# Optimization experiments

Hardware: AMD Instinct MI355X
Metric: run time of the kernel (lower is better)

Reference implementation:

```python
import jax, jax.numpy as jnp
import numpy as np

B, N, D, H, IN, HID = 16, 1024, 256, 8, 256, 1024
HD = IN // H  # head dim = 32
EPS = 1e-5


def layer_norm(x, g, b):
    mu = jnp.mean(x, axis=-1, keepdims=True)
    var = jnp.var(x, axis=-1, keepdims=True)
    return (x - mu) / jnp.sqrt(var + EPS) * g + b


def setup_inputs() -> dict:
    key = jax.random.key(0)
    ks = jax.random.split(key, 12)
    s = 0.02
    return {
        "x": jax.random.normal(ks[0], (B, N, D), jnp.float32),
        "coords": jax.random.normal(ks[1], (B, N, 2), jnp.float32),
        "g1": jnp.ones((D,), jnp.float32),
        "b1": jnp.zeros((D,), jnp.float32),
        "Wqkv": jax.random.normal(ks[2], (3 * IN, D), jnp.float32) * s,
        "Wproj": jax.random.normal(ks[3], (IN, IN), jnp.float32) * s,
        "bproj": jnp.zeros((IN,), jnp.float32),
        "g2": jnp.ones((D,), jnp.float32),
        "b2": jnp.zeros((D,), jnp.float32),
        "W1": jax.random.normal(ks[4], (HID, D), jnp.float32) * s,
        "bb1": jnp.zeros((HID,), jnp.float32),
        "W2": jax.random.normal(ks[5], (D, HID), jnp.float32) * s,
        "bb2": jnp.zeros((D,), jnp.float32),
    }


def reference(x, coords, g1, b1, Wqkv, Wproj, bproj, g2, b2, W1, bb1, W2, bb2):
    # ---- Attention branch (pre-norm) ----
    h = layer_norm(x, g1, b1)                       # [B,N,D]
    qkv = h @ Wqkv.T                                # [B,N,3*IN]
    qkv = qkv.reshape(B, N, 3, H, HD).transpose(2, 0, 3, 1, 4)  # [3,B,H,N,HD]
    q, k, v = qkv[0], qkv[1], qkv[2]
    scale = HD ** -0.5
    attn = jnp.einsum('bhid,bhjd->bhij', q * scale, k)  # [B,H,N,N]
    attn = jax.nn.softmax(attn, axis=-1)
    o = jnp.einsum('bhij,bhjd->bhid', attn, v)      # [B,H,N,HD]
    o = o.transpose(0, 2, 1, 3).reshape(B, N, IN)   # [B,N,IN]
    o = o @ Wproj.T + bproj
    o = o + h                                       # residual inside Attention (vs normed input)
    x = x + o                                       # Block residual (double residual, faithful)
    # ---- MLP branch ----
    h2 = layer_norm(x, g2, b2)
    m = jax.nn.gelu(h2 @ W1.T + bb1, approximate=False) @ W2.T + bb2
    return x + m
```

## Files before the change

### kernel.cpp

```cpp
#include <hip/hip_runtime.h>
#include <hip/hip_bf16.h>
#include <math.h>

#define Bdim 16
#define Ndim 1024
#define Ddim 256
#define Hdim 8
#define HDdim 32
#define INdim 256
#define HIDdim 1024
#define Tdim (Bdim * Ndim)

typedef __attribute__((ext_vector_type(8)))  short bf16x8;
typedef __attribute__((ext_vector_type(4)))  short bf16x4;
typedef __attribute__((ext_vector_type(16))) float f32x16;
typedef unsigned int u32;

__device__ inline short f2bf(float x) {
    union { __hip_bfloat16 b; short s; } u;
    u.b = __float2bfloat16(x);
    return u.s;
}

__device__ inline u32 pack2bf(float a, float b) {
    u32 ua = __float_as_uint(a), ub = __float_as_uint(b);
    return ((ua + 0x8000u) >> 16) | ((ub + 0x8000u) & 0xffff0000u);
}

__device__ inline float gelu_exact(float v) {
    return 0.5f * v * (1.0f + erff(v * 0.70710678118654752f));
}

__global__ __launch_bounds__(256) void cvt_kernel(const float* __restrict__ src,
                                                  short* __restrict__ dst, int n4) {
    int i = blockIdx.x * 256 + threadIdx.x;
    if (i < n4) {
        float4 v = ((const float4*)src)[i];
        bf16x4 b;
        b[0] = f2bf(v.x); b[1] = f2bf(v.y); b[2] = f2bf(v.z); b[3] = f2bf(v.w);
        ((bf16x4*)dst)[i] = b;
    }
}

__global__ __launch_bounds__(256) void ln4_kernel(const float* __restrict__ x,
                                                  const float* __restrict__ g,
                                                  const float* __restrict__ b,
                                                  float* __restrict__ outf,
                                                  short* __restrict__ outb) {
    int w = threadIdx.x >> 6, lane = threadIdx.x & 63;
    int row = blockIdx.x * 4 + w;
    float4 v = ((const float4*)x)[(size_t)row * 64 + lane];
    float s  = (v.x + v.y) + (v.z + v.w);
    float s2 = (v.x * v.x + v.y * v.y) + (v.z * v.z + v.w * v.w);
    #pragma unroll
    for (int off = 32; off; off >>= 1) {
        s  += __shfl_xor(s,  off, 64);
        s2 += __shfl_xor(s2, off, 64);
    }
    float mu   = s * (1.0f / Ddim);
    float var  = s2 * (1.0f / Ddim) - mu * mu;
    float rstd = rsqrtf(var + 1e-5f);
    float4 gg = ((const float4*)g)[lane];
    float4 bb = ((const float4*)b)[lane];
    float4 r;
    r.x = (v.x - mu) * rstd * gg.x + bb.x;
    r.y = (v.y - mu) * rstd * gg.y + bb.y;
    r.z = (v.z - mu) * rstd * gg.z + bb.z;
    r.w = (v.w - mu) * rstd * gg.w + bb.w;
    if (outf) ((float4*)outf)[(size_t)row * 64 + lane] = r;
    bf16x4 rb;
    rb[0] = f2bf(r.x); rb[1] = f2bf(r.y); rb[2] = f2bf(r.z); rb[3] = f2bf(r.w);
    ((bf16x4*)outb)[(size_t)row * 64 + lane] = rb;
}

#define EPI_NONE 0
#define EPI_PROJ 1
#define EPI_GELU 2
#define EPI_RES  3
#define EPI_QKV  4

#define GPAD 40
#define SCALE2Q 0.25505654249892417f

template <int EPI, int BN>
__global__ __launch_bounds__(256) void gemm_mfma(const short* __restrict__ A,
                                                 const short* __restrict__ W,
                                                 void* __restrict__ Cv,
                                                 int M, int N, int K,
                                                 const float* __restrict__ bias,
                                                 const float* __restrict__ add1,
                                                 const float* __restrict__ add2) {
    __shared__ short As[128 * GPAD];
    __shared__ short Bs[BN * GPAD];
    const int tid = threadIdx.x, w = tid >> 6, lane = tid & 63;
    const int col = lane & 31;
    const int half_id = lane >> 5;
    const int m0 = blockIdx.y * 128, n0 = blockIdx.x * BN;
    const int wm = (BN == 128) ? (w & 1) * 64 : w * 32;
    const int wn = (BN == 128) ? (w >> 1) * 64 : 0;
    constexpr int TM = (BN == 128) ? 2 : 1;

    f32x16 acc[TM][2];
    #pragma unroll
    for (int i = 0; i < TM; ++i) { acc[i][0] = 0.0f; acc[i][1] = 0.0f; }

    const int sra = tid >> 1, ssa = (tid & 1) * 2;
    const int srb = (BN == 128) ? (tid >> 1) : (tid >> 2);
    const int ssb = (BN == 128) ? (tid & 1) * 2 : (tid & 3);

    const short* pAsrc = &A[(size_t)(m0 + sra) * K + ssa * 8];
    const short* pBsrc = &W[(size_t)(n0 + srb) * K + ssb * 8];

    bf16x8 pa0, pa1, pb0, pb1;
    pa0 = *(const bf16x8*)&pAsrc[0];
    pa1 = *(const bf16x8*)&pAsrc[8];
    pb0 = *(const bf16x8*)&pBsrc[0];
    if (BN == 128) pb1 = *(const bf16x8*)&pBsrc[8];

    const int T = K >> 5;
    for (int kt = 0; kt < T; ++kt) {
        __syncthreads();
        *(bf16x8*)&As[sra * GPAD + ssa * 8]     = pa0;
        *(bf16x8*)&As[sra * GPAD + ssa * 8 + 8] = pa1;
        *(bf16x8*)&Bs[srb * GPAD + ssb * 8]     = pb0;
        if (BN == 128) *(bf16x8*)&Bs[srb * GPAD + ssb * 8 + 8] = pb1;
        __syncthreads();

        if (kt + 1 < T) {
            const short* a = pAsrc + (kt + 1) * 32;
            const short* b = pBsrc + (kt + 1) * 32;
            pa0 = *(const bf16x8*)&a[0];
            pa1 = *(const bf16x8*)&a[8];
            pb0 = *(const bf16x8*)&b[0];
            if (BN == 128) pb1 = *(const bf16x8*)&b[8];
        }

        #pragma unroll
        for (int ks = 0; ks < 2; ++ks) {
            bf16x8 af[TM], bfv[2];
            #pragma unroll
            for (int t = 0; t < TM; ++t)
                af[t] = *(const bf16x8*)&As[(wm + t * 32 + col) * GPAD + ks * 16 + half_id * 8];
            #pragma unroll
            for (int t = 0; t < 2; ++t)
                bfv[t] = *(const bf16x8*)&Bs[(wn + t * 32 + col) * GPAD + ks * 16 + half_id * 8];
            #pragma unroll
            for (int tm = 0; tm < TM; ++tm)
                #pragma unroll
                for (int tn = 0; tn < 2; ++tn)
                    acc[tm][tn] = __builtin_amdgcn_mfma_f32_32x32x16_bf16(
                        af[tm], bfv[tn], acc[tm][tn], 0, 0, 0);
        }
    }

    float* Cf = (float*)Cv;
    short* Cb = (short*)Cv;
    #pragma unroll
    for (int tm = 0; tm < TM; ++tm) {
        #pragma unroll
        for (int r = 0; r < 16; ++r) {
            int row = m0 + wm + tm * 32 + (r & 3) + 8 * (r >> 2) + 4 * half_id;
            #pragma unroll
            for (int tn = 0; tn < 2; ++tn) {
                int cn = n0 + wn + tn * 32 + col;
                size_t off = (size_t)row * N + cn;
                float v = acc[tm][tn][r];
                if (EPI != EPI_NONE && EPI != EPI_QKV) v += bias[cn];
                if (EPI == EPI_QKV && cn < 256) v *= SCALE2Q;
                if (EPI == EPI_GELU) v = gelu_exact(v);
                if (EPI == EPI_PROJ) v += add1[off] + add2[off];
                if (EPI == EPI_RES)  v += add1[off];
                if (EPI == EPI_PROJ || EPI == EPI_RES) Cf[off] = v;
                else                                   Cb[off] = f2bf(v);
            }
        }
    }
}

#define VTPAD 136

__global__ __launch_bounds__(256) void vtrans_kernel(const short* __restrict__ qkv,
                                                     short* __restrict__ vT) {
    __shared__ short Tl[32 * VTPAD];
    const int tid = threadIdx.x;
    const int bh = blockIdx.x, c = blockIdx.y;
    const int b = bh >> 3, head = bh & 7;
    {
        int r = tid >> 1, hv = tid & 1;
        const short* src = qkv + (size_t)b * Ndim * 768 + (size_t)(c * 128 + r) * 768
                           + 512 + head * 32 + hv * 16;
        bf16x8 v0 = *(const bf16x8*)&src[0];
        bf16x8 v1 = *(const bf16x8*)&src[8];
        #pragma unroll
        for (int i = 0; i < 8; ++i) {
            Tl[(hv * 16 + i) * VTPAD + r]     = v0[i];
            Tl[(hv * 16 + 8 + i) * VTPAD + r] = v1[i];
        }
    }
    __syncthreads();
    {
        int d = tid >> 3, j16 = (tid & 7) * 16;
        short* dst = vT + (size_t)(bh * 32 + d) * Ndim + c * 128 + j16;
        *(bf16x8*)&dst[0] = *(const bf16x8*)&Tl[d * VTPAD + j16];
        *(bf16x8*)&dst[8] = *(const bf16x8*)&Tl[d * VTPAD + j16 + 8];
    }
}

#define KVPAD 40
#define CHUNK 128

__global__ __launch_bounds__(256) void attn_mfma_kernel(const short* __restrict__ qkv,
                                                        const short* __restrict__ vT,
                                                        float* __restrict__ opart,
                                                        float* __restrict__ lpart) {
    __shared__ short Ks[CHUNK * KVPAD];
    __shared__ short Vt[32 * VTPAD];
    __shared__ short Ps[4][2][32 * KVPAD];

    const int tid = threadIdx.x;
    const int w = tid >> 6;
    const int lane = tid & 63;
    const int col = lane & 31;
    const int half_id = lane >> 5;

    const int bh = blockIdx.y;
    const int b = bh >> 3, head = bh & 7;
    const int q0w = blockIdx.x * 128 + w * 32;
    const int part = blockIdx.z;

    const size_t qkvb = (size_t)b * Ndim * 768;
    float* op = opart + (size_t)part * Tdim * 256;
    float* lp = lpart + (size_t)part * Tdim * 8;

    bf16x8 qf[2];
    {
        const short* qrow = qkv + qkvb + (size_t)(q0w + col) * 768 + head * 32;
        #pragma unroll
        for (int kh = 0; kh < 2; ++kh)
            qf[kh] = *(const bf16x8*)&qrow[kh * 16 + half_id * 8];
    }

    bf16x8 vone;
    #pragma unroll
    for (int i = 0; i < 8; ++i) vone[i] = (short)0x3F80;

    f32x16 o_acc = 0.0f, l_acc = 0.0f;

    const int c0 = part * 4;
    for (int c = c0; c < c0 + 4; ++c) {
        if (c != c0) __syncthreads();
        {
            int r = tid >> 1, hv = tid & 1;
            const short* src = qkv + qkvb + (size_t)(c * CHUNK + r) * 768
                               + head * 32 + hv * 16;
            *(bf16x8*)&Ks[r * KVPAD + hv * 16]     = *(const bf16x8*)&src[256];
            *(bf16x8*)&Ks[r * KVPAD + hv * 16 + 8] = *(const bf16x8*)&src[256 + 8];
            int d = tid >> 3, j16 = (tid & 7) * 16;
            const short* vsrc = vT + (size_t)(bh * 32 + d) * Ndim + c * CHUNK + j16;
            *(bf16x8*)&Vt[d * VTPAD + j16]     = *(const bf16x8*)&vsrc[0];
            *(bf16x8*)&Vt[d * VTPAD + j16 + 8] = *(const bf16x8*)&vsrc[8];
        }
        __syncthreads();

        #pragma unroll
        for (int jt = 0; jt < 4; ++jt) {
            short* ps = &Ps[w][jt & 1][0];
            bf16x8 kf0 = *(bf16x8*)&Ks[(jt * 32 + col) * KVPAD + half_id * 8];
            bf16x8 kf1 = *(bf16x8*)&Ks[(jt * 32 + col) * KVPAD + 16 + half_id * 8];
            bf16x8 vf0 = *(bf16x8*)&Vt[col * VTPAD + jt * 32 + half_id * 8];
            bf16x8 vf1 = *(bf16x8*)&Vt[col * VTPAD + jt * 32 + 16 + half_id * 8];

            f32x16 s_acc = 0.0f;
            s_acc = __builtin_amdgcn_mfma_f32_32x32x16_bf16(kf0, qf[0], s_acc, 0, 0, 0);
            s_acc = __builtin_amdgcn_mfma_f32_32x32x16_bf16(kf1, qf[1], s_acc, 0, 0, 0);

            #pragma unroll
            for (int g = 0; g < 4; ++g) {
                float e0 = exp2f(s_acc[g * 4 + 0]);
                float e1 = exp2f(s_acc[g * 4 + 1]);
                float e2 = exp2f(s_acc[g * 4 + 2]);
                float e3 = exp2f(s_acc[g * 4 + 3]);
                uint2 pk;
                pk.x = pack2bf(e0, e1);
                pk.y = pack2bf(e2, e3);
                *(uint2*)&ps[col * KVPAD + g * 8 + half_id * 4] = pk;
            }

            bf16x8 pf0 = *(bf16x8*)&ps[col * KVPAD + half_id * 8];
            bf16x8 pf1 = *(bf16x8*)&ps[col * KVPAD + 16 + half_id * 8];
            o_acc = __builtin_amdgcn_mfma_f32_32x32x16_bf16(pf0, vf0, o_acc, 0, 0, 0);
            o_acc = __builtin_amdgcn_mfma_f32_32x32x16_bf16(pf1, vf1, o_acc, 0, 0, 0);
            l_acc = __builtin_amdgcn_mfma_f32_32x32x16_bf16(pf0, vone, l_acc, 0, 0, 0);
            l_acc = __builtin_amdgcn_mfma_f32_32x32x16_bf16(pf1, vone, l_acc, 0, 0, 0);
        }
    }

    #pragma unroll
    for (int r = 0; r < 16; ++r) {
        int q_r = (r & 3) + 8 * (r >> 2) + 4 * half_id;
        size_t gq = (size_t)(b * Ndim + q0w + q_r);
        op[gq * INdim + head * 32 + col] = o_acc[r];
    }
    if (col < 16) {
        int r = col;
        int q_r = (r & 3) + 8 * (r >> 2) + 4 * half_id;
        lp[(size_t)(b * Ndim + q0w + q_r) * 8 + head] = l_acc[r];
    }
}

__global__ __launch_bounds__(256) void combine_kernel(const float* __restrict__ opart,
                                                      const float* __restrict__ lpart,
                                                      short* __restrict__ oat) {
    int i = blockIdx.x * 256 + threadIdx.x;
    size_t i4 = (size_t)i * 4;
    int gq = (int)(i4 >> 8);
    int head = ((int)(i4 & 255)) >> 5;
    float4 a = ((const float4*)opart)[i];
    float4 b = ((const float4*)(opart + (size_t)Tdim * 256))[i];
    float l = lpart[(size_t)gq * 8 + head] + lpart[(size_t)Tdim * 8 + (size_t)gq * 8 + head];
    float rl = 1.0f / l;
    bf16x4 rb;
    rb[0] = f2bf((a.x + b.x) * rl);
    rb[1] = f2bf((a.y + b.y) * rl);
    rb[2] = f2bf((a.z + b.z) * rl);
    rb[3] = f2bf((a.w + b.w) * rl);
    ((bf16x4*)oat)[i] = rb;
}

extern "C" void kernel_launch(void* const* d_in, const int* in_sizes, int n_in,
                              void* d_out, int out_size, void* d_ws, size_t ws_size,
                              hipStream_t stream) {
    const float* x     = (const float*)d_in[0];
    const float* g1    = (const float*)d_in[2];
    const float* b1    = (const float*)d_in[3];
    const float* Wqkv  = (const float*)d_in[4];
    const float* Wproj = (const float*)d_in[5];
    const float* bproj = (const float*)d_in[6];
    const float* g2    = (const float*)d_in[7];
    const float* b2    = (const float*)d_in[8];
    const float* W1    = (const float*)d_in[9];
    const float* bb1   = (const float*)d_in[10];
    const float* W2    = (const float*)d_in[11];
    const float* bb2   = (const float*)d_in[12];
    float* out = (float*)d_out;

    char* ws = (char*)d_ws;
    float* h      = (float*)(ws);
    short* h_bf   = (short*)(ws + (size_t)(16u << 20));
    short* qkv_bf = (short*)(ws + (size_t)(24u << 20));
    float* xnew   = (float*)(ws + (size_t)(24u << 20));
    short* oat_bf = (short*)(ws + (size_t)(40u << 20));
    float* opart  = (float*)(ws + (size_t)(48u << 20));
    short* mid_bf = (short*)(ws + (size_t)(48u << 20));
    float* lpart  = (float*)(ws + (size_t)(80u << 20));
    short* vT     = (short*)(ws + (size_t)(81u << 20));
    short* wqkv_b = (short*)(ws + (size_t)(89u << 20));
    short* wproj_b= (short*)(ws + (size_t)(89u << 20) + 768 * 1024);
    short* w1_b   = (short*)(ws + (size_t)(90u << 20));
    short* w2_b   = (short*)(ws + (size_t)(90u << 20) + 512 * 1024);

    cvt_kernel<<<(3 * INdim * Ddim / 4 + 255) / 256, 256, 0, stream>>>(Wqkv, wqkv_b, 3 * INdim * Ddim / 4);
    cvt_kernel<<<(INdim * INdim / 4 + 255) / 256, 256, 0, stream>>>(Wproj, wproj_b, INdim * INdim / 4);
    cvt_kernel<<<(HIDdim * Ddim / 4 + 255) / 256, 256, 0, stream>>>(W1, w1_b, HIDdim * Ddim / 4);
    cvt_kernel<<<(Ddim * HIDdim / 4 + 255) / 256, 256, 0, stream>>>(W2, w2_b, Ddim * HIDdim / 4);

    ln4_kernel<<<Tdim / 4, 256, 0, stream>>>(x, g1, b1, h, h_bf);
    gemm_mfma<EPI_QKV, 128><<<dim3(768 / 128, Tdim / 128), 256, 0, stream>>>(
        h_bf, wqkv_b, qkv_bf, Tdim, 768, 256, nullptr, nullptr, nullptr);
    vtrans_kernel<<<dim3(Bdim * Hdim, Ndim / 128), 256, 0, stream>>>(qkv_bf, vT);
    attn_mfma_kernel<<<dim3(Ndim / 128, Bdim * Hdim, 2), 256, 0, stream>>>(
        qkv_bf, vT, opart, lpart);
    combine_kernel<<<(Tdim * INdim / 4) / 256, 256, 0, stream>>>(opart, lpart, oat_bf);
    gemm_mfma<EPI_PROJ, 64><<<dim3(256 / 64, Tdim / 128), 256, 0, stream>>>(
        oat_bf, wproj_b, xnew, Tdim, 256, 256, bproj, h, x);
    ln4_kernel<<<Tdim / 4, 256, 0, stream>>>(xnew, g2, b2, nullptr, h_bf);
    gemm_mfma<EPI_GELU, 128><<<dim3(1024 / 128, Tdim / 128), 256, 0, stream>>>(
        h_bf, w1_b, mid_bf, Tdim, 1024, 256, bb1, nullptr, nullptr);
    gemm_mfma<EPI_RES, 64><<<dim3(256 / 64, Tdim / 128), 256, 0, stream>>>(
        mid_bf, w2_b, out, Tdim, 256, 1024, bb2, xnew, nullptr);
}
```

Measured before the change: 251.4 us.

## Deepen GEMM K-tile, store attention partials in bf16, merge weight casts

The GEMM K-tile doubles from 32 to 64, which halves the number of barrier-synchronised iterations and adds LDS padding to suit. Attention partial outputs are stored as bf16 rather than fp32, cutting write and read traffic for the split-K combine, and the combine kernel now processes 8 elements per thread. The four weight-conversion launches are merged into one kernel, and pack2bf uses the hardware packed bf16 convert when that builtin exists. The trade-offs are extra precision loss on the unnormalised partials and higher LDS and register use per GEMM block.

```diff
diff --git a/kernel.cpp b/kernel.cpp
--- a/kernel.cpp
+++ b/kernel.cpp
@@ -22,24 +22,49 @@
     return u.s;
 }
 
+__device__ inline float bf2f(short s) {
+    return __uint_as_float(((u32)(unsigned short)s) << 16);
+}
+
 __device__ inline u32 pack2bf(float a, float b) {
+#if __has_builtin(__builtin_amdgcn_cvt_pk_bf16_f32)
+    typedef __attribute__((ext_vector_type(2))) __bf16 bf16x2_t;
+    union { bf16x2_t v; u32 u; } c;
+    c.v = __builtin_amdgcn_cvt_pk_bf16_f32(a, b);
+    return c.u;
+#else
     u32 ua = __float_as_uint(a), ub = __float_as_uint(b);
     return ((ua + 0x8000u) >> 16) | ((ub + 0x8000u) & 0xffff0000u);
+#endif
 }
 
 __device__ inline float gelu_exact(float v) {
     return 0.5f * v * (1.0f + erff(v * 0.70710678118654752f));
 }
 
-__global__ __launch_bounds__(256) void cvt_kernel(const float* __restrict__ src,
-                                                  short* __restrict__ dst, int n4) {
+#define N4_QKV  (3 * INdim * Ddim / 4)
+#define N4_PROJ (INdim * INdim / 4)
+#define N4_W1   (HIDdim * Ddim / 4)
+#define N4_W2   (Ddim * HIDdim / 4)
+
+__global__ __launch_bounds__(256) void cvt_all_kernel(const float* __restrict__ s0,
+                                                      const float* __restrict__ s1,
+                                                      const float* __restrict__ s2,
+                                                      const float* __restrict__ s3,
+                                                      short* __restrict__ d0,
+                                                      short* __restrict__ d1,
+                                                      short* __restrict__ d2,
+                                                      short* __restrict__ d3) {
     int i = blockIdx.x * 256 + threadIdx.x;
-    if (i < n4) {
-        float4 v = ((const float4*)src)[i];
-        bf16x4 b;
-        b[0] = f2bf(v.x); b[1] = f2bf(v.y); b[2] = f2bf(v.z); b[3] = f2bf(v.w);
-        ((bf16x4*)dst)[i] = b;
-    }
+    const float* src; short* dst; int j;
+    if (i < N4_QKV)                          { src = s0; dst = d0; j = i; }
+    else if (i < N4_QKV + N4_PROJ)           { src = s1; dst = d1; j = i - N4_QKV; }
+    else if (i < N4_QKV + N4_PROJ + N4_W1)   { src = s2; dst = d2; j = i - N4_QKV - N4_PROJ; }
+    else                                     { src = s3; dst = d3; j = i - N4_QKV - N4_PROJ - N4_W1; }
+    float4 v = ((const float4*)src)[j];
+    bf16x4 b;
+    b[0] = f2bf(v.x); b[1] = f2bf(v.y); b[2] = f2bf(v.z); b[3] = f2bf(v.w);
+    ((bf16x4*)dst)[j] = b;
 }
 
 __global__ __launch_bounds__(256) void ln4_kernel(const float* __restrict__ x,
@@ -79,7 +104,7 @@
 #define EPI_RES  3
 #define EPI_QKV  4
 
-#define GPAD 40
+#define GPAD64 72
 #define SCALE2Q 0.25505654249892417f
 
 template <int EPI, int BN>
@@ -90,8 +115,8 @@
                                                  const float* __restrict__ bias,
                                                  const float* __restrict__ add1,
                                                  const float* __restrict__ add2) {
-    __shared__ short As[128 * GPAD];
-    __shared__ short Bs[BN * GPAD];
+    __shared__ short As[128 * GPAD64];
+    __shared__ short Bs[BN * GPAD64];
     const int tid = threadIdx.x, w = tid >> 6, lane = tid & 63;
     const int col = lane & 31;
     const int half_id = lane >> 5;
@@ -104,46 +129,47 @@
     #pragma unroll
     for (int i = 0; i < TM; ++i) { acc[i][0] = 0.0f; acc[i][1] = 0.0f; }
 
-    const int sra = tid >> 1, ssa = (tid & 1) * 2;
+    const int sra = tid >> 1, ssa = (tid & 1) * 32;
     const int srb = (BN == 128) ? (tid >> 1) : (tid >> 2);
-    const int ssb = (BN == 128) ? (tid & 1) * 2 : (tid & 3);
-
-    const short* pAsrc = &A[(size_t)(m0 + sra) * K + ssa * 8];
-    const short* pBsrc = &W[(size_t)(n0 + srb) * K + ssb * 8];
-
-    bf16x8 pa0, pa1, pb0, pb1;
-    pa0 = *(const bf16x8*)&pAsrc[0];
-    pa1 = *(const bf16x8*)&pAsrc[8];
-    pb0 = *(const bf16x8*)&pBsrc[0];
-    if (BN == 128) pb1 = *(const bf16x8*)&pBsrc[8];
-
-    const int T = K >> 5;
+    const int ssb = (BN == 128) ? (tid & 1) * 32 : (tid & 3) * 16;
+    constexpr int NB = (BN == 128) ? 4 : 2;
+
+    const short* pAsrc = &A[(size_t)(m0 + sra) * K + ssa];
+    const short* pBsrc = &W[(size_t)(n0 + srb) * K + ssb];
+
+    bf16x8 pa[4], pb[NB];
+    #pragma unroll
+    for (int j = 0; j < 4; ++j) pa[j] = *(const bf16x8*)&pAsrc[j * 8];
+    #pragma unroll
+    for (int j = 0; j < NB; ++j) pb[j] = *(const bf16x8*)&pBsrc[j * 8];
+
+    const int T = K >> 6;
     for (int kt = 0; kt < T; ++kt) {
         __syncthreads();
-        *(bf16x8*)&As[sra * GPAD + ssa * 8]     = pa0;
-        *(bf16x8*)&As[sra * GPAD + ssa * 8 + 8] = pa1;
-        *(bf16x8*)&Bs[srb * GPAD + ssb * 8]     = pb0;
-        if (BN == 128) *(bf16x8*)&Bs[srb * GPAD + ssb * 8 + 8] = pb1;
+        #pragma unroll
+        for (int j = 0; j < 4; ++j) *(bf16x8*)&As[sra * GPAD64 + ssa + j * 8] = pa[j];
+        #pragma unroll
+        for (int j = 0; j < NB; ++j) *(bf16x8*)&Bs[srb * GPAD64 + ssb + j * 8] = pb[j];
         __syncthreads();
 
         if (kt + 1 < T) {
-            const short* a = pAsrc + (kt + 1) * 32;
-            const short* b = pBsrc + (kt + 1) * 32;
-            pa0 = *(const bf16x8*)&a[0];
-            pa1 = *(const bf16x8*)&a[8];
-            pb0 = *(const bf16x8*)&b[0];
-            if (BN == 128) pb1 = *(const bf16x8*)&b[8];
-        }
-
-        #pragma unroll
-        for (int ks = 0; ks < 2; ++ks) {
+            const short* a = pAsrc + (kt + 1) * 64;
+            const short* b = pBsrc + (kt + 1) * 64;
+            #pragma unroll
+            for (int j = 0; j < 4; ++j) pa[j] = *(const bf16x8*)&a[j * 8];
+            #pragma unroll
+            for (int j = 0; j < NB; ++j) pb[j] = *(const bf16x8*)&b[j * 8];
+        }
+
+        #pragma unroll
+        for (int ks = 0; ks < 4; ++ks) {
             bf16x8 af[TM], bfv[2];
             #pragma unroll
             for (int t = 0; t < TM; ++t)
-                af[t] = *(const bf16x8*)&As[(wm + t * 32 + col) * GPAD + ks * 16 + half_id * 8];
+                af[t] = *(const bf16x8*)&As[(wm + t * 32 + col) * GPAD64 + ks * 16 + half_id * 8];
             #pragma unroll
             for (int t = 0; t < 2; ++t)
-                bfv[t] = *(const bf16x8*)&Bs[(wn + t * 32 + col) * GPAD + ks * 16 + half_id * 8];
+                bfv[t] = *(const bf16x8*)&Bs[(wn + t * 32 + col) * GPAD64 + ks * 16 + half_id * 8];
             #pragma unroll
             for (int tm = 0; tm < TM; ++tm)
                 #pragma unroll
@@ -211,7 +237,7 @@
 
 __global__ __launch_bounds__(256) void attn_mfma_kernel(const short* __restrict__ qkv,
                                                         const short* __restrict__ vT,
-                                                        float* __restrict__ opart,
+                                                        short* __restrict__ opart,
                                                         float* __restrict__ lpart) {
     __shared__ short Ks[CHUNK * KVPAD];
     __shared__ short Vt[32 * VTPAD];
@@ -229,7 +255,7 @@
     const int part = blockIdx.z;
 
     const size_t qkvb = (size_t)b * Ndim * 768;
-    float* op = opart + (size_t)part * Tdim * 256;
+    short* op = opart + (size_t)part * Tdim * 256;
     float* lp = lpart + (size_t)part * Tdim * 8;
 
     bf16x8 qf[2];
@@ -299,7 +325,7 @@
     for (int r = 0; r < 16; ++r) {
         int q_r = (r & 3) + 8 * (r >> 2) + 4 * half_id;
         size_t gq = (size_t)(b * Ndim + q0w + q_r);
-        op[gq * INdim + head * 32 + col] = o_acc[r];
+        op[gq * INdim + head * 32 + col] = f2bf(o_acc[r]);
     }
     if (col < 16) {
         int r = col;
@@ -308,23 +334,21 @@
     }
 }
 
-__global__ __launch_bounds__(256) void combine_kernel(const float* __restrict__ opart,
+__global__ __launch_bounds__(256) void combine_kernel(const short* __restrict__ opart,
                                                       const float* __restrict__ lpart,
                                                       short* __restrict__ oat) {
     int i = blockIdx.x * 256 + threadIdx.x;
-    size_t i4 = (size_t)i * 4;
-    int gq = (int)(i4 >> 8);
-    int head = ((int)(i4 & 255)) >> 5;
-    float4 a = ((const float4*)opart)[i];
-    float4 b = ((const float4*)(opart + (size_t)Tdim * 256))[i];
+    size_t base = (size_t)i * 8;
+    int gq = (int)(base >> 8);
+    int head = ((int)(base & 255)) >> 5;
+    bf16x8 a = ((const bf16x8*)opart)[i];
+    bf16x8 b = ((const bf16x8*)(opart + (size_t)Tdim * 256))[i];
     float l = lpart[(size_t)gq * 8 + head] + lpart[(size_t)Tdim * 8 + (size_t)gq * 8 + head];
     float rl = 1.0f / l;
-    bf16x4 rb;
-    rb[0] = f2bf((a.x + b.x) * rl);
-    rb[1] = f2bf((a.y + b.y) * rl);
-    rb[2] = f2bf((a.z + b.z) * rl);
-    rb[3] = f2bf((a.w + b.w) * rl);
-    ((bf16x4*)oat)[i] = rb;
+    bf16x8 r;
+    #pragma unroll
+    for (int j = 0; j < 8; ++j) r[j] = f2bf((bf2f(a[j]) + bf2f(b[j])) * rl);
+    ((bf16x8*)oat)[i] = r;
 }
 
 extern "C" void kernel_launch(void* const* d_in, const int* in_sizes, int n_in,
@@ -350,7 +374,7 @@
     short* qkv_bf = (short*)(ws + (size_t)(24u << 20));
     float* xnew   = (float*)(ws + (size_t)(24u << 20));
     short* oat_bf = (short*)(ws + (size_t)(40u << 20));
-    float* opart  = (float*)(ws + (size_t)(48u << 20));
+    short* opart  = (short*)(ws + (size_t)(48u << 20));
     short* mid_bf = (short*)(ws + (size_t)(48u << 20));
     float* lpart  = (float*)(ws + (size_t)(80u << 20));
     short* vT     = (short*)(ws + (size_t)(81u << 20));
@@ -359,10 +383,8 @@
     short* w1_b   = (short*)(ws + (size_t)(90u << 20));
     short* w2_b   = (short*)(ws + (size_t)(90u << 20) + 512 * 1024);
 
-    cvt_kernel<<<(3 * INdim * Ddim / 4 + 255) / 256, 256, 0, stream>>>(Wqkv, wqkv_b, 3 * INdim * Ddim / 4);
-    cvt_kernel<<<(INdim * INdim / 4 + 255) / 256, 256, 0, stream>>>(Wproj, wproj_b, INdim * INdim / 4);
-    cvt_kernel<<<(HIDdim * Ddim / 4 + 255) / 256, 256, 0, stream>>>(W1, w1_b, HIDdim * Ddim / 4);
-    cvt_kernel<<<(Ddim * HIDdim / 4 + 255) / 256, 256, 0, stream>>>(W2, w2_b, Ddim * HIDdim / 4);
+    cvt_all_kernel<<<(N4_QKV + N4_PROJ + N4_W1 + N4_W2 + 255) / 256, 256, 0, stream>>>(
+        Wqkv, Wproj, W1, W2, wqkv_b, wproj_b, w1_b, w2_b);
 
     ln4_kernel<<<Tdim / 4, 256, 0, stream>>>(x, g1, b1, h, h_bf);
     gemm_mfma<EPI_QKV, 128><<<dim3(768 / 128, Tdim / 128), 256, 0, stream>>>(
@@ -370,7 +392,7 @@
     vtrans_kernel<<<dim3(Bdim * Hdim, Ndim / 128), 256, 0, stream>>>(qkv_bf, vT);
     attn_mfma_kernel<<<dim3(Ndim / 128, Bdim * Hdim, 2), 256, 0, stream>>>(
         qkv_bf, vT, opart, lpart);
-    combine_kernel<<<(Tdim * INdim / 4) / 256, 256, 0, stream>>>(opart, lpart, oat_bf);
+    combine_kernel<<<(Tdim * INdim / 8) / 256, 256, 0, stream>>>(opart, lpart, oat_bf);
     gemm_mfma<EPI_PROJ, 64><<<dim3(256 / 64, Tdim / 128), 256, 0, stream>>>(
         oat_bf, wproj_b, xnew, Tdim, 256, 256, bproj, h, x);
     ln4_kernel<<<Tdim / 4, 256, 0, stream>>>(xnew, g2, b2, nullptr, h_bf);
```

Measured after the change: 237.7 us. -5.5%, faster.
